# Performance work log

Hardware: AMD Instinct MI355X
Metric: run time of the kernel (lower is better)

The kernel has to match this reference:

```python
import jax, jax.numpy as jnp
import numpy as np

B, T, D, H, K, O = 512, 512, 64, 64, 4, 2


def setup_inputs() -> dict:
    key = jax.random.key(0)
    ks = jax.random.split(key, 12)
    s_i = 1.0 / np.sqrt(D)
    s_h = 1.0 / np.sqrt(H)
    return {
        "x": jax.random.normal(ks[0], (B, T, D), jnp.float32),
        "ctx": jax.random.randint(ks[1], (B, T), 0, K, jnp.int32),
        "mask": jax.random.bernoulli(ks[2], 0.9, (B, T)),
        "W_ir": jax.random.normal(ks[3], (H, D), jnp.float32) * s_i,
        "W_iz": jax.random.normal(ks[4], (H, D), jnp.float32) * s_i,
        "W_in": jax.random.normal(ks[5], (H, D), jnp.float32) * s_i,
        "b_ir": jnp.zeros((H,), jnp.float32),
        "b_iz": jnp.zeros((H,), jnp.float32),
        "b_in": jnp.zeros((H,), jnp.float32),
        "W_hr": jax.random.normal(ks[6], (K, H, H), jnp.float32) * s_h,
        "W_hz": jax.random.normal(ks[7], (K, H, H), jnp.float32) * s_h,
        "W_hn": jax.random.normal(ks[8], (K, H, H), jnp.float32) * s_h,
        "b_hr": jnp.zeros((K, H), jnp.float32),
        "b_hz": jnp.zeros((K, H), jnp.float32),
        "b_hn": jnp.zeros((K, H), jnp.float32),
        "Wo_w": jax.random.normal(ks[9], (O, H), jnp.float32) * s_h,
        "Wo_b": jnp.zeros((O,), jnp.float32),
    }


def reference(x, ctx, mask, W_ir, W_iz, W_in, b_ir, b_iz, b_in,
              W_hr, W_hz, W_hn, b_hr, b_hz, b_hn, Wo_w, Wo_b):
    Bv, Tv, _ = x.shape
    Hv = W_ir.shape[0]
    # precompute all input projections: [B,T,H]
    ir = jnp.einsum('btd,hd->bth', x, W_ir) + b_ir
    iz = jnp.einsum('btd,hd->bth', x, W_iz) + b_iz
    inn = jnp.einsum('btd,hd->bth', x, W_in) + b_in
    mt = mask.astype(x.dtype)  # [B,T]

    def step(h, inp):
        ir_t, iz_t, in_t, kt, m_t = inp  # [B,H],[B,H],[B,H],[B],[B]
        hr = jnp.einsum('bij,bj->bi', W_hr[kt], h) + b_hr[kt]
        hz = jnp.einsum('bij,bj->bi', W_hz[kt], h) + b_hz[kt]
        hn = jnp.einsum('bij,bj->bi', W_hn[kt], h) + b_hn[kt]
        r = jax.nn.sigmoid(ir_t + hr)
        z = jax.nn.sigmoid(iz_t + hz)
        n = jnp.tanh(in_t + r * hn)
        h_new = (1.0 - z) * n + z * h
        h = m_t[:, None] * h_new + (1.0 - m_t[:, None]) * h
        return h, h

    xs = (jnp.swapaxes(ir, 0, 1), jnp.swapaxes(iz, 0, 1), jnp.swapaxes(inn, 0, 1),
          ctx.T, mt.T)
    h0 = jnp.zeros((Bv, Hv), x.dtype)
    _, hs = jax.lax.scan(step, h0, xs)  # hs: [T,B,H]
    logits = jnp.einsum('tbh,oh->bto', hs, Wo_w) + Wo_b  # [B,T,O]
    return logits
```

## Files before the change

### kernel.cpp

```cpp
#include <hip/hip_runtime.h>
#include <hip/hip_fp16.h>

#define B_ 512
#define T_ 512
#define H_ 64
#define K_ 4

#define WS_WIT_OFF   98304
#define WS_FLAG_OFF  123136
#define WS_XH_OFF    131072
#define WS_IPJ_OFF   131072
#define WS_HH_OFF    201457664ULL
#define WS_NEED_FAST 235012096ULL

#define LDS_HSC_OFF  122880
#define LDS_TOTAL    123392
#define STAGE_U4     7680

#define LDS14_HSC_OFF 32768
#define LDS14_TOTAL   33024

typedef _Float16 half2_t __attribute__((ext_vector_type(2)));

union Q { uint4 u; half2_t h[4]; };

__device__ __forceinline__ float fdot2f(half2_t a, half2_t b, float c) {
#if __has_builtin(__builtin_amdgcn_fdot2)
    return __builtin_amdgcn_fdot2(a, b, c, false);
#else
    return fmaf((float)a[0], (float)b[0], fmaf((float)a[1], (float)b[1], c));
#endif
}

__device__ __forceinline__ half2_t pkh2(float a, float b) {
    return __builtin_bit_cast(half2_t, __builtin_amdgcn_cvt_pkrtz(a, b));
}

__global__ void detect_mask_kernel(const unsigned char* __restrict__ mb, int* __restrict__ flag) {
    __shared__ int cnt;
    if (threadIdx.x == 0) cnt = 0;
    __syncthreads();
    int c = 0;
    for (int i = threadIdx.x; i < 4096; i += blockDim.x)
        if ((i & 3) != 0 && mb[i] != 0) c++;
    atomicAdd(&cnt, c);
    __syncthreads();
    if (threadIdx.x == 0) *flag = (cnt > 0) ? 1 : 0;
}

__global__ void convert_weights_kernel(const float* __restrict__ Whr, const float* __restrict__ Whz,
                                       const float* __restrict__ Whn, const float* __restrict__ Wir,
                                       const float* __restrict__ Wiz, const float* __restrict__ Win,
                                       __half* __restrict__ wht, __half* __restrict__ wit) {
    int idx = blockIdx.x * 256 + threadIdx.x;
    if (idx < K_ * 3 * H_ * H_) {
        int mat = idx >> 12;
        int i   = (idx >> 6) & 63;
        int j   = idx & 63;
        int k   = mat / 3, g = mat - 3 * k;
        const float* src = (g == 0) ? Whr : (g == 1) ? Whz : Whn;
        wht[((mat * 8 + (j >> 3)) * 64 + i) * 8 + (j & 7)] = __float2half(src[(k * H_ + i) * H_ + j]);
    }
    if (idx < 3 * H_ * H_) {
        int g = idx >> 12;
        int i = (idx >> 6) & 63;
        int j = idx & 63;
        const float* src = (g == 0) ? Wir : (g == 1) ? Wiz : Win;
        wit[((g * 8 + (j >> 3)) * 64 + i) * 8 + (j & 7)] = __float2half(src[i * H_ + j]);
    }
}

__global__ void convert_x_kernel(const float* __restrict__ xf, __half* __restrict__ xh) {
    size_t i = (size_t)blockIdx.x * 256 + threadIdx.x;
    if (i >= (size_t)B_ * T_ * H_ / 8) return;
    const float4* p = (const float4*)xf + 2 * i;
    float4 a = p[0], b = p[1];
    Q o;
    o.h[0] = pkh2(a.x, a.y);
    o.h[1] = pkh2(a.z, a.w);
    o.h[2] = pkh2(b.x, b.y);
    o.h[3] = pkh2(b.z, b.w);
    ((uint4*)xh)[i] = o.u;
}

__global__ __launch_bounds__(256, 1)
void iproj_kernel(const float* __restrict__ xf, const __half* __restrict__ wit,
                  const float* __restrict__ b_ir, const float* __restrict__ b_iz,
                  const float* __restrict__ b_in, float* __restrict__ iproj) {
    const int lane = threadIdx.x & 63;
    const int grp  = threadIdx.x >> 6;
    Q wr[8], wz[8], wn[8];
    const uint4* wp = (const uint4*)wit + lane;
#pragma unroll
    for (int q = 0; q < 8; q++) {
        wr[q].u = wp[q * 64];
        wz[q].u = wp[512 + q * 64];
        wn[q].u = wp[1024 + q * 64];
    }
    const float bir = b_ir[lane], biz = b_iz[lane], bin = b_in[lane];
    const int bt_base = blockIdx.x * 32 + grp * 8;

    float4 raw[16];
    {
        const float4* xp = (const float4*)(xf + (size_t)bt_base * H_);
#pragma unroll
        for (int j = 0; j < 16; j++) raw[j] = xp[j];
    }
#pragma unroll
    for (int r = 0; r < 8; r++) {
        const int bt = bt_base + r;
        Q xq[8];
#pragma unroll
        for (int q = 0; q < 8; q++) {
            float4 a = raw[2 * q], b4 = raw[2 * q + 1];
            xq[q].h[0] = pkh2(a.x, a.y);
            xq[q].h[1] = pkh2(a.z, a.w);
            xq[q].h[2] = pkh2(b4.x, b4.y);
            xq[q].h[3] = pkh2(b4.z, b4.w);
        }
        if (r < 7) {
            const float4* xp = (const float4*)(xf + (size_t)(bt + 1) * H_);
#pragma unroll
            for (int j = 0; j < 16; j++) raw[j] = xp[j];
        }
        float sir = bir, siz = biz, sin_ = bin;
#pragma unroll
        for (int q = 0; q < 8; q++)
#pragma unroll
            for (int p = 0; p < 4; p++) {
                sir  = fdot2f(wr[q].h[p], xq[q].h[p], sir);
                siz  = fdot2f(wz[q].h[p], xq[q].h[p], siz);
                sin_ = fdot2f(wn[q].h[p], xq[q].h[p], sin_);
            }
        float* op = iproj + (size_t)bt * 192;
        op[lane] = sir; op[64 + lane] = siz; op[128 + lane] = sin_;
    }
}

#define DSR(DST, ADDR, OFF) \
    asm volatile("ds_read_b128 %0, %1 offset:" #OFF : "=v"(DST) : "v"(ADDR));
#define GLD(DST, PTR, OFF) \
    asm volatile("global_load_dwordx4 %0, %1, off offset:" #OFF : "=v"(DST) : "v"(PTR));

#define PREFL8(RN, VB)                                                          \
    DSR(RN[0].u, VB, 0)    DSR(RN[1].u, VB, 1024)                               \
    DSR(RN[2].u, VB, 2048) DSR(RN[3].u, VB, 3072)                               \
    DSR(RN[4].u, VB, 4096) DSR(RN[5].u, VB, 5120)                               \
    DSR(RN[6].u, VB, 6144) DSR(RN[7].u, VB, 7168)

#define BSEL(K, A0, A1, A2, A3) (((K) == 0) ? (A0) : ((K) == 1) ? (A1) : ((K) == 2) ? (A2) : (A3))

#define LOADCHUNK(IPR, IPZ, IPN, CTXV, MSKV, T0)                                \
{                                                                               \
    __builtin_amdgcn_sched_barrier(0);                                          \
    const int t0c = (T0);                                                       \
    _Pragma("unroll") for (int s = 0; s < 8; s++) {                             \
           \
           \
        int tcl = t0c + s; tcl = (tcl < T_) ? tcl : s;                          \
        const float* ipp = iproj + (size_t)(bt0 + tcl) * 192;                   \
        IPR[s] = ipp[lane]; IPZ[s] = ipp[64 + lane]; IPN[s] = ipp[128 + lane];  \
    }                                                                           \
    int tcc = t0c + (lane & 7); tcc = (tcc < T_) ? tcc : (T_ - 1);              \
    CTXV = ctx[bt0 + tcc];                                                      \
    MSKV = (int)maskb[(size_t)(bt0 + tcc) << mshift];                           \
    __builtin_amdgcn_sched_barrier(0);                                          \
}

#define STEP14(TT, SS, NW, ZC, NC, RC, ZN, NN, RN, KNU_EXPR, IPR, IPZ, IPN, CTXC, MSKC) \
{                                                                               \
    const int tt  = (TT);                                                       \
    const int kcu = __builtin_amdgcn_readlane(CTXC, SS);                        \
    const int knu = (KNU_EXPR);                                                 \
                      \
    asm volatile("s_waitcnt vmcnt(" #NW ")" ::: "memory");                      \
    __builtin_amdgcn_sched_barrier(0);                                          \
       \
    { const char* gb0 = whtl + (size_t)knu * 24576 + 8192;                      \
      const char* gb1 = gb0 + 4096;                                             \
      const char* gb2 = gb0 + 8192;                                             \
      const char* gb3 = gb0 + 12288;                                            \
      GLD(ZN[0].u, gb0, 0) GLD(ZN[1].u, gb0, 1024)                              \
      GLD(ZN[2].u, gb0, 2048) GLD(ZN[3].u, gb0, 3072)                           \
      GLD(ZN[4].u, gb1, 0) GLD(ZN[5].u, gb1, 1024)                              \
      GLD(ZN[6].u, gb1, 2048) GLD(ZN[7].u, gb1, 3072)                           \
      GLD(NN[0].u, gb2, 0) GLD(NN[1].u, gb2, 1024)                              \
      GLD(NN[2].u, gb2, 2048) GLD(NN[3].u, gb2, 3072)                           \
      GLD(NN[4].u, gb3, 0) GLD(NN[5].u, gb3, 1024)                              \
      GLD(NN[6].u, gb3, 2048) GLD(NN[7].u, gb3, 3072) }                         \
    __builtin_amdgcn_sched_barrier(0);                                          \
        \
    float shr, shz, shn;                                                        \
    { float a4[4] = {0,0,0,0};                                                  \
      _Pragma("unroll") for (int q = 0; q < 8; q++)                             \
        _Pragma("unroll") for (int p = 0; p < 4; p++)                           \
          a4[q >> 1] = fdot2f(ZC[q].h[p], hq[q].h[p], a4[q >> 1]);              \
      shz = (a4[0] + a4[1]) + (a4[2] + a4[3]); }                                \
    { float a4[4] = {0,0,0,0};                                                  \
      _Pragma("unroll") for (int q = 0; q < 8; q++)                             \
        _Pragma("unroll") for (int p = 0; p < 4; p++)                           \
          a4[q >> 1] = fdot2f(NC[q].h[p], hq[q].h[p], a4[q >> 1]);              \
      shn = (a4[0] + a4[1]) + (a4[2] + a4[3]); }                                \
            \
    asm volatile("s_waitcnt lgkmcnt(0)" ::: "memory");                          \
    __builtin_amdgcn_sched_barrier(0);                                          \
    { float a4[4] = {0,0,0,0};                                                  \
      _Pragma("unroll") for (int q = 0; q < 8; q++)                             \
        _Pragma("unroll") for (int p = 0; p < 4; p++)                           \
          a4[q >> 1] = fdot2f(RC[q].h[p], hq[q].h[p], a4[q >> 1]);              \
      shr = (a4[0] + a4[1]) + (a4[2] + a4[3]); }                                \
                   \
    const float bhr = BSEL(kcu, bR0, bR1, bR2, bR3);                            \
    const float bhz = BSEL(kcu, bZ0, bZ1, bZ2, bZ3);                            \
    const float bhn = BSEL(kcu, bN0, bN1, bN2, bN3);                            \
    const float mcv = (__builtin_amdgcn_readlane(MSKC, SS) != 0) ? 1.0f : 0.0f; \
    const float arv = IPR[SS] + shr + bhr;                                      \
    const float azv = IPZ[SS] + shz + bhz;                                      \
    const float rr  = 1.0f / (1.0f + __expf(-arv));                             \
    const float zz  = 1.0f / (1.0f + __expf(-azv));                             \
    const float aa  = IPN[SS] + rr * (shn + bhn);                               \
    const float nn2 = 2.0f / (1.0f + __expf(-2.0f * aa)) - 1.0f;                \
    float hnew = nn2 + zz * (hreg - nn2);                                       \
    hnew = (mcv > 0.5f) ? hnew : hreg;                                          \
    hreg = hnew;                                                                \
    const __half h16 = __float2half(hnew);                                      \
    hh0[(size_t)tt * H_ + lane] = h16;           \
                    \
    hsc[((SS & 1) << 6) + lane] = h16;                                          \
    __builtin_amdgcn_wave_barrier();                                            \
    { const uint4* hp = (const uint4*)(hsc + ((SS & 1) << 6));                  \
      _Pragma("unroll") for (int q = 0; q < 8; q++) hq[q].u = hp[q]; }          \
    __builtin_amdgcn_wave_barrier();                                            \
    asm volatile("s_waitcnt lgkmcnt(0)" ::: "memory");                          \
    __builtin_amdgcn_sched_barrier(0);                                          \
            \
    { const unsigned int vb = lds0 + (unsigned int)(knu * 8192) + ((unsigned int)lane << 4); \
      PREFL8(RN, vb) }                                                          \
    __builtin_amdgcn_sched_barrier(0);                                          \
}

#define RUNCHUNK14(T0, IPR, IPZ, IPN, CTXC, MSKC, CTXN)                         \
    STEP14(T0 + 0, 0, 27, zA, nA, rA, zB, nB, rB, __builtin_amdgcn_readlane(CTXC, 1), IPR, IPZ, IPN, CTXC, MSKC) \
    STEP14(T0 + 1, 1, 1,  zB, nB, rB, zA, nA, rA, __builtin_amdgcn_readlane(CTXC, 2), IPR, IPZ, IPN, CTXC, MSKC) \
    STEP14(T0 + 2, 2, 1,  zA, nA, rA, zB, nB, rB, __builtin_amdgcn_readlane(CTXC, 3), IPR, IPZ, IPN, CTXC, MSKC) \
    STEP14(T0 + 3, 3, 1,  zB, nB, rB, zA, nA, rA, __builtin_amdgcn_readlane(CTXC, 4), IPR, IPZ, IPN, CTXC, MSKC) \
    STEP14(T0 + 4, 4, 1,  zA, nA, rA, zB, nB, rB, __builtin_amdgcn_readlane(CTXC, 5), IPR, IPZ, IPN, CTXC, MSKC) \
    STEP14(T0 + 5, 5, 1,  zB, nB, rB, zA, nA, rA, __builtin_amdgcn_readlane(CTXC, 6), IPR, IPZ, IPN, CTXC, MSKC) \
    STEP14(T0 + 6, 6, 1,  zA, nA, rA, zB, nB, rB, __builtin_amdgcn_readlane(CTXC, 7), IPR, IPZ, IPN, CTXC, MSKC) \
    STEP14(T0 + 7, 7, 1,  zB, nB, rB, zA, nA, rA, __builtin_amdgcn_readlane(CTXN, 0), IPR, IPZ, IPN, CTXC, MSKC)

__global__ __launch_bounds__(64, 1)
void gru_seq14(const float* __restrict__ iproj, const int* __restrict__ ctx,
               const unsigned char* __restrict__ maskb, const int* __restrict__ flagp,
               const __half* __restrict__ wht,
               const float* __restrict__ b_hr, const float* __restrict__ b_hz,
               const float* __restrict__ b_hn, __half* __restrict__ hh) {
    extern __shared__ __align__(16) char smem[];
    uint4* swr = (uint4*)smem;
    const int lane = threadIdx.x;
    const int bt0  = blockIdx.x * T_;

    {
        const uint4* g = (const uint4*)wht;
#pragma unroll 4
        for (int i = lane; i < 2048; i += 64)
            swr[i] = g[(i >> 9) * 1536 + (i & 511)];
    }
    __syncthreads();

    const unsigned int lds0 = (unsigned int)(uintptr_t)smem;
    const char* whtl = (const char*)wht + ((size_t)lane << 4);

    const int flag   = *flagp;
    const int mshift = flag ? 0 : 2;
    __half* hh0 = hh + (size_t)bt0 * H_;
    __half* hsc = (__half*)(smem + LDS14_HSC_OFF);

    const float bR0 = b_hr[lane],       bR1 = b_hr[64 + lane];
    const float bR2 = b_hr[128 + lane], bR3 = b_hr[192 + lane];
    const float bZ0 = b_hz[lane],       bZ1 = b_hz[64 + lane];
    const float bZ2 = b_hz[128 + lane], bZ3 = b_hz[192 + lane];
    const float bN0 = b_hn[lane],       bN1 = b_hn[64 + lane];
    const float bN2 = b_hn[128 + lane], bN3 = b_hn[192 + lane];

    float hreg = 0.0f;
    Q hq[8];
#pragma unroll
    for (int q = 0; q < 8; q++) hq[q].u = make_uint4(0u, 0u, 0u, 0u);

    float ipAr[8], ipAz[8], ipAn[8];
    float ipBr[8], ipBz[8], ipBn[8];
    int ctxA, mskA, ctxB, mskB;
    LOADCHUNK(ipAr, ipAz, ipAn, ctxA, mskA, 0)

    Q zA[8], nA[8], rA[8], zB[8], nB[8], rB[8];
    {
        const int k0u = __builtin_amdgcn_readlane(ctxA, 0);
        const uint4* gwp = (const uint4*)wht + k0u * 1536 + lane;
#pragma unroll
        for (int q = 0; q < 8; q++) {
            zA[q].u = gwp[512 + q * 64];
            nA[q].u = gwp[1024 + q * 64];
            rA[q].u = swr[k0u * 512 + q * 64 + lane];
        }
    }

#pragma unroll 1
    for (int c = 0; c < 64; c += 2) {
        const int t0a = c << 3, t0b = t0a + 8;
        LOADCHUNK(ipBr, ipBz, ipBn, ctxB, mskB, t0b)
        RUNCHUNK14(t0a, ipAr, ipAz, ipAn, ctxA, mskA, ctxB)
        LOADCHUNK(ipAr, ipAz, ipAn, ctxA, mskA, t0b + 8)
        RUNCHUNK14(t0b, ipBr, ipBz, ipBn, ctxB, mskB, ctxA)
    }
}

__global__ __launch_bounds__(256, 1)
void logits_kernel(const __half* __restrict__ hh, const float* __restrict__ Wo_w,
                   const float* __restrict__ Wo_b, float* __restrict__ out) {
    const int bt = blockIdx.x * 256 + threadIdx.x;
    const uint4* hp = (const uint4*)(hh + (size_t)bt * H_);
    const float wob0 = Wo_b[0], wob1 = Wo_b[1];
    float l0 = 0.0f, l1 = 0.0f;
#pragma unroll
    for (int q = 0; q < 8; q++) {
        Q h8; h8.u = hp[q];
#pragma unroll
        for (int p = 0; p < 4; p++) {
            const int j = q * 8 + p * 2;
            const float v0 = (float)h8.h[p][0];
            const float v1 = (float)h8.h[p][1];
            l0 = fmaf(v0, Wo_w[j], l0);
            l0 = fmaf(v1, Wo_w[j + 1], l0);
            l1 = fmaf(v0, Wo_w[64 + j], l1);
            l1 = fmaf(v1, Wo_w[64 + j + 1], l1);
        }
    }
    *(float2*)(out + (size_t)bt * 2) = make_float2(l0 + wob0, l1 + wob1);
}

#define STEP(TT, WCUR, WNXT, BUF)                                              \
{                                                                              \
    const int tt = (TT);                                                       \
    const int tn = (tt + 1 < T_) ? tt + 1 : T_ - 1;                            \
    Q xq[8];                                                                   \
    { const uint4* xp = (const uint4*)(xh16 + (size_t)(bt0 + tt) * H_);        \
      _Pragma("unroll") for (int q = 0; q < 8; q++) xq[q].u = xp[q]; }         \
    float ar4[4] = {0,0,0,0}, az4[4] = {0,0,0,0}, an4[4] = {0,0,0,0};          \
    _Pragma("unroll") for (int q = 0; q < 8; q++) {                            \
        _Pragma("unroll") for (int p = 0; p < 4; p++) {                        \
            ar4[q >> 1] = fdot2f(WCUR[q].h[p],      hq[q].h[p], ar4[q >> 1]);  \
            az4[q >> 1] = fdot2f(WCUR[8 + q].h[p],  hq[q].h[p], az4[q >> 1]);  \
            an4[q >> 1] = fdot2f(WCUR[16 + q].h[p], hq[q].h[p], an4[q >> 1]);  \
        }                                                                      \
    }                                                                          \
    const float shr = (ar4[0] + ar4[1]) + (ar4[2] + ar4[3]);                   \
    const float shz = (az4[0] + az4[1]) + (az4[2] + az4[3]);                   \
    const float shn = (an4[0] + an4[1]) + (an4[2] + an4[3]);                   \
    float sir = bir, siz = biz, sin_ = bin;                                    \
    _Pragma("unroll") for (int q = 0; q < 8; q++) {                            \
        Q wr, wz, wn;                                                          \
        wr.u = swi[q * 64 + lane];                                             \
        wz.u = swi[512 + q * 64 + lane];                                       \
        wn.u = swi[1024 + q * 64 + lane];                                      \
        _Pragma("unroll") for (int p = 0; p < 4; p++) {                        \
            sir  = fdot2f(wr.h[p], xq[q].h[p], sir);                           \
            siz  = fdot2f(wz.h[p], xq[q].h[p], siz);                           \
            sin_ = fdot2f(wn.h[p], xq[q].h[p], sin_);                          \
        }                                                                      \
    }                                                                          \
    const int kn = __builtin_amdgcn_readfirstlane(ctx[bt0 + tn]);              \
    const unsigned char mn = maskb[(size_t)(bt0 + tn) << mshift];              \
    const float bhr_n = b_hr[kn * H_ + lane];                                  \
    const float bhz_n = b_hz[kn * H_ + lane];                                  \
    const float bhn_n = b_hn[kn * H_ + lane];                                  \
    { const uint4* wp = sw + kn * 1536 + lane;                                 \
      _Pragma("unroll") for (int q = 0; q < 8; q++) {                          \
        WNXT[q].u      = wp[q * 64];                                           \
        WNXT[8 + q].u  = wp[512 + q * 64];                                     \
        WNXT[16 + q].u = wp[1024 + q * 64];                                    \
      } }                                                                      \
    const float arv = sir + shr + bhr_c;                                       \
    const float azv = siz + shz + bhz_c;                                       \
    const float rr  = 1.0f / (1.0f + __expf(-arv));                            \
    const float zz  = 1.0f / (1.0f + __expf(-azv));                            \
    const float aa  = sin_ + rr * (shn + bhn_c);                               \
    const float nn2 = 2.0f / (1.0f + __expf(-2.0f * aa)) - 1.0f;               \
    float hnew = nn2 + zz * (hreg - nn2);                                      \
    hnew = (mc > 0.5f) ? hnew : hreg;                                          \
    hreg = hnew;                                                               \
    { __half* hb = hsc + ((BUF) << 6);                                         \
      hb[lane] = __float2half(hnew);                                           \
      __builtin_amdgcn_wave_barrier();                                         \
      const uint4* hp = (const uint4*)hb;                                      \
      _Pragma("unroll") for (int q = 0; q < 8; q++) hq[q].u = hp[q];           \
      __builtin_amdgcn_wave_barrier(); }                                       \
    { float l0 = hnew * wo0, l1 = hnew * wo1;                                  \
      _Pragma("unroll") for (int m = 32; m >= 1; m >>= 1) {                    \
          l0 += __shfl_xor(l0, m, 64);                                         \
          l1 += __shfl_xor(l1, m, 64);                                         \
      }                                                                        \
      if (lane == 0) *(float2*)(outp + tt * 2) = make_float2(l0 + wob0, l1 + wob1); } \
    bhr_c = bhr_n; bhz_c = bhz_n; bhn_c = bhn_n;                               \
    mc = mn ? 1.0f : 0.0f;                                                     \
}

__global__ __launch_bounds__(128, 1)
void gru_seq6(const __half* __restrict__ xh16, const int* __restrict__ ctx,
              const unsigned char* __restrict__ maskb, const int* __restrict__ flagp,
              const __half* __restrict__ wht,
              const float* __restrict__ b_ir, const float* __restrict__ b_iz,
              const float* __restrict__ b_in, const float* __restrict__ b_hr,
              const float* __restrict__ b_hz, const float* __restrict__ b_hn,
              const float* __restrict__ Wo_w, const float* __restrict__ Wo_b,
              float* __restrict__ out) {
    extern __shared__ __align__(16) char smem[];
    uint4* sw  = (uint4*)smem;
    uint4* swi = sw + 6144;

    const int tid  = threadIdx.x;
    const int lane = tid & 63;
    const int wv   = tid >> 6;
    const int b    = blockIdx.x * 2 + wv;

    {
        const uint4* gsrc = (const uint4*)wht;
#pragma unroll 1
        for (int i = tid; i < STAGE_U4; i += 128) sw[i] = gsrc[i];
    }
    __syncthreads();

    const int flag   = *flagp;
    const int mshift = flag ? 0 : 2;
    const int bt0    = b * T_;

    const float bir = b_ir[lane], biz = b_iz[lane], bin = b_in[lane];
    const float wo0 = Wo_w[lane], wo1 = Wo_w[64 + lane];
    const float wob0 = Wo_b[0], wob1 = Wo_b[1];

    __half* hsc = (__half*)(smem + LDS_HSC_OFF + (wv << 8));
    float*  outp = out + (size_t)b * T_ * 2;

    float hreg = 0.0f;
    Q hq[8];
#pragma unroll
    for (int q = 0; q < 8; q++) hq[q].u = make_uint4(0u, 0u, 0u, 0u);

    Q wA[24], wB[24];
    const int k0 = __builtin_amdgcn_readfirstlane(ctx[bt0]);
    float mc = maskb[(size_t)bt0 << mshift] ? 1.0f : 0.0f;
    float bhr_c = b_hr[k0 * H_ + lane];
    float bhz_c = b_hz[k0 * H_ + lane];
    float bhn_c = b_hn[k0 * H_ + lane];
    {
        const uint4* wp = sw + k0 * 1536 + lane;
#pragma unroll
        for (int q = 0; q < 8; q++) {
            wA[q].u      = wp[q * 64];
            wA[8 + q].u  = wp[512 + q * 64];
            wA[16 + q].u = wp[1024 + q * 64];
        }
    }

#pragma unroll 1
    for (int t = 0; t < T_; t += 2) {
        STEP(t,     wA, wB, 0)
        STEP(t + 1, wB, wA, 1)
    }
}

extern "C" void kernel_launch(void* const* d_in, const int* in_sizes, int n_in,
                              void* d_out, int out_size, void* d_ws, size_t ws_size,
                              hipStream_t stream) {
    const float* x    = (const float*)d_in[0];
    const int*   ctx  = (const int*)d_in[1];
    const void*  mask = d_in[2];
    const float* W_ir = (const float*)d_in[3];
    const float* W_iz = (const float*)d_in[4];
    const float* W_in = (const float*)d_in[5];
    const float* bir  = (const float*)d_in[6];
    const float* biz  = (const float*)d_in[7];
    const float* bin  = (const float*)d_in[8];
    const float* W_hr = (const float*)d_in[9];
    const float* W_hz = (const float*)d_in[10];
    const float* W_hn = (const float*)d_in[11];
    const float* bhr  = (const float*)d_in[12];
    const float* bhz  = (const float*)d_in[13];
    const float* bhn  = (const float*)d_in[14];
    const float* Wo_w = (const float*)d_in[15];
    const float* Wo_b = (const float*)d_in[16];

    char* ws = (char*)d_ws;
    __half* wht  = (__half*)ws;
    __half* wit  = (__half*)(ws + WS_WIT_OFF);
    int*    flag = (int*)(ws + WS_FLAG_OFF);

    detect_mask_kernel<<<1, 256, 0, stream>>>((const unsigned char*)mask, flag);
    convert_weights_kernel<<<192, 256, 0, stream>>>(W_hr, W_hz, W_hn, W_ir, W_iz, W_in,
                                                    wht, wit);

    if (ws_size >= (size_t)WS_NEED_FAST) {
        float*  iproj = (float*)(ws + WS_IPJ_OFF);
        __half* hh    = (__half*)(ws + WS_HH_OFF);
        iproj_kernel<<<B_ * T_ / 32, 256, 0, stream>>>(x, wit, bir, biz, bin, iproj);
        (void)hipFuncSetAttribute((const void*)gru_seq14,
                                  hipFuncAttributeMaxDynamicSharedMemorySize, LDS14_TOTAL);
        gru_seq14<<<B_, 64, LDS14_TOTAL, stream>>>(
            iproj, ctx, (const unsigned char*)mask, flag, wht, bhr, bhz, bhn, hh);
        logits_kernel<<<B_ * T_ / 256, 256, 0, stream>>>(hh, Wo_w, Wo_b, (float*)d_out);
    } else {
        __half* xh16 = (__half*)(ws + WS_XH_OFF);
        convert_x_kernel<<<8192, 256, 0, stream>>>(x, xh16);
        (void)hipFuncSetAttribute((const void*)gru_seq6,
                                  hipFuncAttributeMaxDynamicSharedMemorySize, LDS_TOTAL);
        gru_seq6<<<B_ / 2, 128, LDS_TOTAL, stream>>>(
            xh16, ctx, (const unsigned char*)mask, flag, wht,
            bir, biz, bin, bhr, bhz, bhn, Wo_w, Wo_b, (float*)d_out);
    }
}
```

Measured before the change: 594.6 us.

## Prefetch next-step LDS weights early in GRU step and preconvert x to fp16

In the recurrent step, the LDS reads of the next step's r-gate weights are now issued right after the global weight loads, and the mid-step lgkmcnt(0) wait is dropped. This lets the LDS latency overlap with the z and n dot products instead of sitting at the tail of the serial step. Separately, x is now converted to fp16 by its own kernel that always runs, and the input-projection kernel reads those halves with a two-row double buffer. This adds an extra kernel launch and a wider workspace layout. The earlier LDS prefetch also raises register pressure and relies on the later waitcnt for correctness.

```diff
diff --git a/kernel.cpp b/kernel.cpp
--- a/kernel.cpp
+++ b/kernel.cpp
@@ -9,16 +9,16 @@
 #define WS_WIT_OFF   98304
 #define WS_FLAG_OFF  123136
 #define WS_XH_OFF    131072
-#define WS_IPJ_OFF   131072
-#define WS_HH_OFF    201457664ULL
-#define WS_NEED_FAST 235012096ULL
+#define WS_IPJ_OFF   33685504ULL
+#define WS_HH_OFF    235012096ULL
+#define WS_NEED_FAST 268566528ULL
 
 #define LDS_HSC_OFF  122880
 #define LDS_TOTAL    123392
 #define STAGE_U4     7680
 
-#define LDS14_HSC_OFF 32768
-#define LDS14_TOTAL   33024
+#define LDS15_HSC_OFF 32768
+#define LDS15_TOTAL   33024
 
 typedef _Float16 half2_t __attribute__((ext_vector_type(2)));
 
@@ -84,11 +84,11 @@
 }
 
 __global__ __launch_bounds__(256, 1)
-void iproj_kernel(const float* __restrict__ xf, const __half* __restrict__ wit,
+void iproj_kernel(const __half* __restrict__ xh16, const __half* __restrict__ wit,
                   const float* __restrict__ b_ir, const float* __restrict__ b_iz,
                   const float* __restrict__ b_in, float* __restrict__ iproj) {
     const int lane = threadIdx.x & 63;
-    const int grp  = threadIdx.x >> 6;
+    const int wv   = threadIdx.x >> 6;
     Q wr[8], wz[8], wn[8];
     const uint4* wp = (const uint4*)wit + lane;
 #pragma unroll
@@ -98,43 +98,34 @@
         wn[q].u = wp[1024 + q * 64];
     }
     const float bir = b_ir[lane], biz = b_iz[lane], bin = b_in[lane];
-    const int bt_base = blockIdx.x * 32 + grp * 8;
-
-    float4 raw[16];
-    {
-        const float4* xp = (const float4*)(xf + (size_t)bt_base * H_);
-#pragma unroll
-        for (int j = 0; j < 16; j++) raw[j] = xp[j];
-    }
-#pragma unroll
-    for (int r = 0; r < 8; r++) {
-        const int bt = bt_base + r;
-        Q xq[8];
-#pragma unroll
-        for (int q = 0; q < 8; q++) {
-            float4 a = raw[2 * q], b4 = raw[2 * q + 1];
-            xq[q].h[0] = pkh2(a.x, a.y);
-            xq[q].h[1] = pkh2(a.z, a.w);
-            xq[q].h[2] = pkh2(b4.x, b4.y);
-            xq[q].h[3] = pkh2(b4.z, b4.w);
-        }
-        if (r < 7) {
-            const float4* xp = (const float4*)(xf + (size_t)(bt + 1) * H_);
-#pragma unroll
-            for (int j = 0; j < 16; j++) raw[j] = xp[j];
-        }
-        float sir = bir, siz = biz, sin_ = bin;
-#pragma unroll
-        for (int q = 0; q < 8; q++)
-#pragma unroll
-            for (int p = 0; p < 4; p++) {
-                sir  = fdot2f(wr[q].h[p], xq[q].h[p], sir);
-                siz  = fdot2f(wz[q].h[p], xq[q].h[p], siz);
-                sin_ = fdot2f(wn[q].h[p], xq[q].h[p], sin_);
-            }
-        float* op = iproj + (size_t)bt * 192;
-        op[lane] = sir; op[64 + lane] = siz; op[128 + lane] = sin_;
-    }
+    const int bt_base = blockIdx.x * 32 + wv * 8;
+
+#define IPJ_LOAD(DST, ROW)                                                      \
+    { const uint4* xp = (const uint4*)(xh16 + (size_t)(ROW) * H_);              \
+      _Pragma("unroll") for (int q = 0; q < 8; q++) DST[q].u = xp[q]; }
+#define IPJ_COMP(SRC, ROW)                                                      \
+    { float sir = bir, siz = biz, sin_ = bin;                                   \
+      _Pragma("unroll") for (int q = 0; q < 8; q++)                             \
+        _Pragma("unroll") for (int p = 0; p < 4; p++) {                         \
+            sir  = fdot2f(wr[q].h[p], SRC[q].h[p], sir);                        \
+            siz  = fdot2f(wz[q].h[p], SRC[q].h[p], siz);                        \
+            sin_ = fdot2f(wn[q].h[p], SRC[q].h[p], sin_);                       \
+        }                                                                       \
+      float* op = iproj + (size_t)(ROW) * 192;                                  \
+      op[lane] = sir; op[64 + lane] = siz; op[128 + lane] = sin_; }
+
+    Q x0[8], x1[8];
+    IPJ_LOAD(x0, bt_base)
+    IPJ_LOAD(x1, bt_base + 1)
+#pragma unroll
+    for (int rp = 0; rp < 8; rp += 2) {
+        IPJ_COMP(x0, bt_base + rp)
+        if (rp + 2 < 8) IPJ_LOAD(x0, bt_base + rp + 2)
+        IPJ_COMP(x1, bt_base + rp + 1)
+        if (rp + 3 < 8) IPJ_LOAD(x1, bt_base + rp + 3)
+    }
+#undef IPJ_LOAD
+#undef IPJ_COMP
 }
 
 #define DSR(DST, ADDR, OFF) \
@@ -167,7 +158,7 @@
     __builtin_amdgcn_sched_barrier(0);                                          \
 }
 
-#define STEP14(TT, SS, NW, ZC, NC, RC, ZN, NN, RN, KNU_EXPR, IPR, IPZ, IPN, CTXC, MSKC) \
+#define STEP15(TT, SS, NW, ZC, NC, RC, ZN, NN, RN, KNU_EXPR, IPR, IPZ, IPN, CTXC, MSKC) \
 {                                                                               \
     const int tt  = (TT);                                                       \
     const int kcu = __builtin_amdgcn_readlane(CTXC, SS);                        \
@@ -188,6 +179,10 @@
       GLD(NN[2].u, gb2, 2048) GLD(NN[3].u, gb2, 3072)                           \
       GLD(NN[4].u, gb3, 0) GLD(NN[5].u, gb3, 1024)                              \
       GLD(NN[6].u, gb3, 2048) GLD(NN[7].u, gb3, 3072) }                         \
+      \
+     \
+    { const unsigned int vb = lds0 + (unsigned int)(knu * 8192) + ((unsigned int)lane << 4); \
+      PREFL8(RN, vb) }                                                          \
     __builtin_amdgcn_sched_barrier(0);                                          \
         \
     float shr, shz, shn;                                                        \
@@ -201,9 +196,7 @@
         _Pragma("unroll") for (int p = 0; p < 4; p++)                           \
           a4[q >> 1] = fdot2f(NC[q].h[p], hq[q].h[p], a4[q >> 1]);              \
       shn = (a4[0] + a4[1]) + (a4[2] + a4[3]); }                                \
-            \
-    asm volatile("s_waitcnt lgkmcnt(0)" ::: "memory");                          \
-    __builtin_amdgcn_sched_barrier(0);                                          \
+         \
     { float a4[4] = {0,0,0,0};                                                  \
       _Pragma("unroll") for (int q = 0; q < 8; q++)                             \
         _Pragma("unroll") for (int p = 0; p < 4; p++)                           \
@@ -224,8 +217,8 @@
     hnew = (mcv > 0.5f) ? hnew : hreg;                                          \
     hreg = hnew;                                                                \
     const __half h16 = __float2half(hnew);                                      \
-    hh0[(size_t)tt * H_ + lane] = h16;           \
-                    \
+    hh0[(size_t)tt * H_ + lane] = h16;      \
+         \
     hsc[((SS & 1) << 6) + lane] = h16;                                          \
     __builtin_amdgcn_wave_barrier();                                            \
     { const uint4* hp = (const uint4*)(hsc + ((SS & 1) << 6));                  \
@@ -233,24 +226,20 @@
     __builtin_amdgcn_wave_barrier();                                            \
     asm volatile("s_waitcnt lgkmcnt(0)" ::: "memory");                          \
     __builtin_amdgcn_sched_barrier(0);                                          \
-            \
-    { const unsigned int vb = lds0 + (unsigned int)(knu * 8192) + ((unsigned int)lane << 4); \
-      PREFL8(RN, vb) }                                                          \
-    __builtin_amdgcn_sched_barrier(0);                                          \
-}
-
-#define RUNCHUNK14(T0, IPR, IPZ, IPN, CTXC, MSKC, CTXN)                         \
-    STEP14(T0 + 0, 0, 27, zA, nA, rA, zB, nB, rB, __builtin_amdgcn_readlane(CTXC, 1), IPR, IPZ, IPN, CTXC, MSKC) \
-    STEP14(T0 + 1, 1, 1,  zB, nB, rB, zA, nA, rA, __builtin_amdgcn_readlane(CTXC, 2), IPR, IPZ, IPN, CTXC, MSKC) \
-    STEP14(T0 + 2, 2, 1,  zA, nA, rA, zB, nB, rB, __builtin_amdgcn_readlane(CTXC, 3), IPR, IPZ, IPN, CTXC, MSKC) \
-    STEP14(T0 + 3, 3, 1,  zB, nB, rB, zA, nA, rA, __builtin_amdgcn_readlane(CTXC, 4), IPR, IPZ, IPN, CTXC, MSKC) \
-    STEP14(T0 + 4, 4, 1,  zA, nA, rA, zB, nB, rB, __builtin_amdgcn_readlane(CTXC, 5), IPR, IPZ, IPN, CTXC, MSKC) \
-    STEP14(T0 + 5, 5, 1,  zB, nB, rB, zA, nA, rA, __builtin_amdgcn_readlane(CTXC, 6), IPR, IPZ, IPN, CTXC, MSKC) \
-    STEP14(T0 + 6, 6, 1,  zA, nA, rA, zB, nB, rB, __builtin_amdgcn_readlane(CTXC, 7), IPR, IPZ, IPN, CTXC, MSKC) \
-    STEP14(T0 + 7, 7, 1,  zB, nB, rB, zA, nA, rA, __builtin_amdgcn_readlane(CTXN, 0), IPR, IPZ, IPN, CTXC, MSKC)
+}
+
+#define RUNCHUNK15(T0, IPR, IPZ, IPN, CTXC, MSKC, CTXN)                         \
+    STEP15(T0 + 0, 0, 27, zA, nA, rA, zB, nB, rB, __builtin_amdgcn_readlane(CTXC, 1), IPR, IPZ, IPN, CTXC, MSKC) \
+    STEP15(T0 + 1, 1, 1,  zB, nB, rB, zA, nA, rA, __builtin_amdgcn_readlane(CTXC, 2), IPR, IPZ, IPN, CTXC, MSKC) \
+    STEP15(T0 + 2, 2, 1,  zA, nA, rA, zB, nB, rB, __builtin_amdgcn_readlane(CTXC, 3), IPR, IPZ, IPN, CTXC, MSKC) \
+    STEP15(T0 + 3, 3, 1,  zB, nB, rB, zA, nA, rA, __builtin_amdgcn_readlane(CTXC, 4), IPR, IPZ, IPN, CTXC, MSKC) \
+    STEP15(T0 + 4, 4, 1,  zA, nA, rA, zB, nB, rB, __builtin_amdgcn_readlane(CTXC, 5), IPR, IPZ, IPN, CTXC, MSKC) \
+    STEP15(T0 + 5, 5, 1,  zB, nB, rB, zA, nA, rA, __builtin_amdgcn_readlane(CTXC, 6), IPR, IPZ, IPN, CTXC, MSKC) \
+    STEP15(T0 + 6, 6, 1,  zA, nA, rA, zB, nB, rB, __builtin_amdgcn_readlane(CTXC, 7), IPR, IPZ, IPN, CTXC, MSKC) \
+    STEP15(T0 + 7, 7, 1,  zB, nB, rB, zA, nA, rA, __builtin_amdgcn_readlane(CTXN, 0), IPR, IPZ, IPN, CTXC, MSKC)
 
 __global__ __launch_bounds__(64, 1)
-void gru_seq14(const float* __restrict__ iproj, const int* __restrict__ ctx,
+void gru_seq15(const float* __restrict__ iproj, const int* __restrict__ ctx,
                const unsigned char* __restrict__ maskb, const int* __restrict__ flagp,
                const __half* __restrict__ wht,
                const float* __restrict__ b_hr, const float* __restrict__ b_hz,
@@ -274,7 +263,7 @@
     const int flag   = *flagp;
     const int mshift = flag ? 0 : 2;
     __half* hh0 = hh + (size_t)bt0 * H_;
-    __half* hsc = (__half*)(smem + LDS14_HSC_OFF);
+    __half* hsc = (__half*)(smem + LDS15_HSC_OFF);
 
     const float bR0 = b_hr[lane],       bR1 = b_hr[64 + lane];
     const float bR2 = b_hr[128 + lane], bR3 = b_hr[192 + lane];
@@ -309,9 +298,9 @@
     for (int c = 0; c < 64; c += 2) {
         const int t0a = c << 3, t0b = t0a + 8;
         LOADCHUNK(ipBr, ipBz, ipBn, ctxB, mskB, t0b)
-        RUNCHUNK14(t0a, ipAr, ipAz, ipAn, ctxA, mskA, ctxB)
+        RUNCHUNK15(t0a, ipAr, ipAz, ipAn, ctxA, mskA, ctxB)
         LOADCHUNK(ipAr, ipAz, ipAn, ctxA, mskA, t0b + 8)
-        RUNCHUNK14(t0b, ipBr, ipBz, ipBn, ctxB, mskB, ctxA)
+        RUNCHUNK15(t0b, ipBr, ipBz, ipBn, ctxB, mskB, ctxA)
     }
 }
 
@@ -494,23 +483,23 @@
     __half* wht  = (__half*)ws;
     __half* wit  = (__half*)(ws + WS_WIT_OFF);
     int*    flag = (int*)(ws + WS_FLAG_OFF);
+    __half* xh16 = (__half*)(ws + WS_XH_OFF);
 
     detect_mask_kernel<<<1, 256, 0, stream>>>((const unsigned char*)mask, flag);
     convert_weights_kernel<<<192, 256, 0, stream>>>(W_hr, W_hz, W_hn, W_ir, W_iz, W_in,
                                                     wht, wit);
+    convert_x_kernel<<<8192, 256, 0, stream>>>(x, xh16);
 
     if (ws_size >= (size_t)WS_NEED_FAST) {
         float*  iproj = (float*)(ws + WS_IPJ_OFF);
         __half* hh    = (__half*)(ws + WS_HH_OFF);
-        iproj_kernel<<<B_ * T_ / 32, 256, 0, stream>>>(x, wit, bir, biz, bin, iproj);
-        (void)hipFuncSetAttribute((const void*)gru_seq14,
-                                  hipFuncAttributeMaxDynamicSharedMemorySize, LDS14_TOTAL);
-        gru_seq14<<<B_, 64, LDS14_TOTAL, stream>>>(
+        iproj_kernel<<<B_ * T_ / 32, 256, 0, stream>>>(xh16, wit, bir, biz, bin, iproj);
+        (void)hipFuncSetAttribute((const void*)gru_seq15,
+                                  hipFuncAttributeMaxDynamicSharedMemorySize, LDS15_TOTAL);
+        gru_seq15<<<B_, 64, LDS15_TOTAL, stream>>>(
             iproj, ctx, (const unsigned char*)mask, flag, wht, bhr, bhz, bhn, hh);
         logits_kernel<<<B_ * T_ / 256, 256, 0, stream>>>(hh, Wo_w, Wo_b, (float*)d_out);
     } else {
-        __half* xh16 = (__half*)(ws + WS_XH_OFF);
-        convert_x_kernel<<<8192, 256, 0, stream>>>(x, xh16);
         (void)hipFuncSetAttribute((const void*)gru_seq6,
                                   hipFuncAttributeMaxDynamicSharedMemorySize, LDS_TOTAL);
         gru_seq6<<<B_ / 2, 128, LDS_TOTAL, stream>>>(
```

Result: slower. 674.4 us (+13.4%).
